# Kernel tuning notes

Hardware: AMD Instinct MI355X
Metric: run time of the kernel (lower is better)

The kernel has to match this reference:

```python
import jax, jax.numpy as jnp
import numpy as np

P = 16  # patch_size

def setup_inputs() -> dict:
    key = jax.random.key(0)
    k1, k2, k3, k4, k5 = jax.random.split(key, 5)
    B, C, H, W = 8, 256, 256, 256
    x = jax.random.normal(k1, (B, C, H, W), dtype=jnp.float32)
    w1 = jax.random.normal(k2, (C, C), dtype=jnp.float32) * 0.02
    b1 = jax.random.normal(k3, (C,), dtype=jnp.float32) * 0.02
    w2 = jax.random.normal(k4, (C, C), dtype=jnp.float32) * 0.02
    b2 = jax.random.normal(k5, (C,), dtype=jnp.float32) * 0.02
    return {"x": x, "w1": w1, "b1": b1, "w2": w2, "b2": b2}

def reference(x, w1, b1, w2, b2):
    B, C, H, W = x.shape
    h, w = H // P, W // P
    # global feature: mean over all spatial positions -> (B, C)
    gf = jnp.mean(x, axis=(2, 3))
    # local features: per-patch mean -> (B, C, h, w)
    lf = jnp.mean(x.reshape(B, C, h, P, w, P), axis=(3, 5))
    lf = lf.reshape(B, C, h * w).transpose(0, 2, 1)  # (B, hw, C)
    mix = jnp.concatenate([lf, gf[:, None, :]], axis=1)  # (B, hw+1, C)
    m = jax.nn.relu(jnp.einsum('bnc,oc->bno', mix, w1) + b1)
    m = jax.nn.relu(jnp.einsum('bnc,oc->bno', m, w2) + b2)
    lf2, gf2 = m[:, :-1, :], m[:, -1, :]  # (B, hw, C), (B, C)
    scores = jnp.einsum('bnc,bc->bn', lf2, gf2)  # (B, hw)
    att = jax.nn.softmax(scores, axis=1).reshape(B, 1, h, w)
    # upsample attention over each patch (nearest / block-broadcast)
    att_up = jnp.repeat(jnp.repeat(att, P, axis=2), P, axis=3)  # (B,1,H,W)
    return x + x * att_up
```

## Files before the change

### kernel.cpp

```cpp
#include <hip/hip_runtime.h>
#include <hip/hip_bf16.h>

typedef float f32x4 __attribute__((ext_vector_type(4)));

#define WS_W1T 0
#define WS_W2T 65536
#define WS_MIX 131072
#define WS_M2  657408
#define WS_ATT 1183744

__global__ void k_transpose(const float* __restrict__ w1,
                            const float* __restrict__ w2,
                            float* __restrict__ w1t,
                            float* __restrict__ w2t) {
    int t = blockIdx.x * 256 + threadIdx.x;
    int idx = t & 65535;
    int o = idx >> 8, c = idx & 255;
    if (t < 65536) w1t[c * 256 + o] = w1[idx];
    else           w2t[c * 256 + o] = w2[idx];
}

__global__ void k_patch_means(const float* __restrict__ x,
                              float* __restrict__ mix) {
    int plane = blockIdx.x;
    int b = plane >> 8, c = plane & 255;
    const f32x4* p = (const f32x4*)x + (size_t)plane * 16384;
    int t = threadIdx.x;
    int lane = t & 63, wid = t >> 6;
    int pcol = lane >> 2;

    __shared__ float bins[16][16];

    const f32x4* wp = p + (size_t)wid * 64 * 64 + lane;
    for (int band = 0; band < 4; ++band) {
        float acc = 0.f;
        #pragma unroll
        for (int r = 0; r < 16; ++r) {
            f32x4 v = __builtin_nontemporal_load(wp + (band * 16 + r) * 64);
            acc += v.x + v.y + v.z + v.w;
        }
        acc += __shfl_xor(acc, 1);
        acc += __shfl_xor(acc, 2);
        if ((lane & 3) == 0) bins[wid * 4 + band][pcol] = acc;
    }
    __syncthreads();

    float pm = bins[t >> 4][t & 15] * (1.0f / 256.0f);
    mix[((size_t)b * 257 + t) * 256 + c] = pm;

    float s = pm;
    for (int off = 1; off < 64; off <<= 1) s += __shfl_xor(s, off);
    __shared__ float wsum[4];
    if (lane == 0) wsum[wid] = s;
    __syncthreads();
    if (t == 0) {
        float g = (wsum[0] + wsum[1] + wsum[2] + wsum[3]) * (1.0f / 256.0f);
        mix[((size_t)b * 257 + 256) * 256 + c] = g;
    }
}

__global__ void k_mlp(const float* __restrict__ mix,
                      const float* __restrict__ w1t, const float* __restrict__ b1,
                      const float* __restrict__ w2t, const float* __restrict__ b2,
                      float* __restrict__ m2out) {
    int r0 = blockIdx.x * 4;
    int o = threadIdx.x;

    __shared__ float in[4][256];
    __shared__ float mid[4][256];
    #pragma unroll
    for (int j = 0; j < 4; ++j) in[j][o] = mix[(size_t)(r0 + j) * 256 + o];
    __syncthreads();

    float acc[4];
    float bb = b1[o];
    #pragma unroll
    for (int j = 0; j < 4; ++j) acc[j] = bb;
    #pragma unroll 4
    for (int c = 0; c < 256; ++c) {
        float wv = w1t[c * 256 + o];
        #pragma unroll
        for (int j = 0; j < 4; ++j) acc[j] = fmaf(in[j][c], wv, acc[j]);
    }
    #pragma unroll
    for (int j = 0; j < 4; ++j) mid[j][o] = fmaxf(acc[j], 0.f);
    __syncthreads();

    float bb2 = b2[o];
    #pragma unroll
    for (int j = 0; j < 4; ++j) acc[j] = bb2;
    #pragma unroll 4
    for (int c = 0; c < 256; ++c) {
        float wv = w2t[c * 256 + o];
        #pragma unroll
        for (int j = 0; j < 4; ++j) acc[j] = fmaf(mid[j][c], wv, acc[j]);
    }
    #pragma unroll
    for (int j = 0; j < 4; ++j)
        m2out[(size_t)(r0 + j) * 256 + o] = fmaxf(acc[j], 0.f);
}

__global__ void k_softmax(const float* __restrict__ m2,
                          float* __restrict__ att) {
    int b = blockIdx.x;
    const float* base = m2 + (size_t)b * 257 * 256;
    int t = threadIdx.x;
    int lane = t & 63, w = t >> 6;

    __shared__ float gf2[256];
    __shared__ float scores[256];
    if (t < 256) gf2[t] = base[65536 + t];
    __syncthreads();

    f32x4 gv = ((const f32x4*)gf2)[lane];
    for (int r = 0; r < 16; ++r) {
        int n = w * 16 + r;
        f32x4 v = ((const f32x4*)(base + (size_t)n * 256))[lane];
        float s = v.x * gv.x + v.y * gv.y + v.z * gv.z + v.w * gv.w;
        #pragma unroll
        for (int off = 1; off < 64; off <<= 1) s += __shfl_xor(s, off);
        if (lane == 0) scores[n] = s;
    }
    __syncthreads();

    float s = (t < 256) ? scores[t] : -1e30f;
    float m = s;
    #pragma unroll
    for (int off = 1; off < 64; off <<= 1) m = fmaxf(m, __shfl_xor(m, off));
    __shared__ float redm[16];
    if (lane == 0) redm[w] = m;
    __syncthreads();
    float M = fmaxf(fmaxf(redm[0], redm[1]), fmaxf(redm[2], redm[3]));

    float e = (t < 256) ? __expf(s - M) : 0.f;
    float sum = e;
    #pragma unroll
    for (int off = 1; off < 64; off <<= 1) sum += __shfl_xor(sum, off);
    __shared__ float reds[16];
    if (lane == 0) reds[w] = sum;
    __syncthreads();
    float S = reds[0] + reds[1] + reds[2] + reds[3];

    if (t < 256) att[b * 256 + t] = e / S;
}

__global__ void k_apply(const float* __restrict__ x,
                        const float* __restrict__ att,
                        float* __restrict__ out) {
    const f32x4* xv = (const f32x4*)x;
    f32x4* ov = (f32x4*)out;
    size_t base = (size_t)blockIdx.x * 1024 + threadIdx.x;
    #pragma unroll
    for (int k = 0; k < 4; ++k) {
        size_t i = base + (size_t)k * 256;
        int plane = (int)(i >> 14);
        int j = (int)(i & 16383);
        int row = j >> 6, col4 = j & 63;
        int patch = ((row >> 4) << 4) | (col4 >> 2);
        int b = plane >> 8;
        float a = 1.0f + att[(b << 8) + patch];
        f32x4 v = __builtin_nontemporal_load(&xv[i]);
        v.x *= a; v.y *= a; v.z *= a; v.w *= a;
        __builtin_nontemporal_store(v, &ov[i]);
    }
}

extern "C" void kernel_launch(void* const* d_in, const int* in_sizes, int n_in,
                              void* d_out, int out_size, void* d_ws, size_t ws_size,
                              hipStream_t stream) {
    const float* x  = (const float*)d_in[0];
    const float* w1 = (const float*)d_in[1];
    const float* b1 = (const float*)d_in[2];
    const float* w2 = (const float*)d_in[3];
    const float* b2 = (const float*)d_in[4];
    float* out = (float*)d_out;
    float* ws  = (float*)d_ws;

    float* w1t = ws + WS_W1T;
    float* w2t = ws + WS_W2T;
    float* mix = ws + WS_MIX;
    float* m2  = ws + WS_M2;
    float* att = ws + WS_ATT;

    k_transpose<<<512, 256, 0, stream>>>(w1, w2, w1t, w2t);
    k_patch_means<<<8 * 256, 256, 0, stream>>>(x, mix);
    k_mlp<<<(8 * 257) / 4, 256, 0, stream>>>(mix, w1t, b1, w2t, b2, m2);
    k_softmax<<<8, 1024, 0, stream>>>(m2, att);
    k_apply<<<32768, 256, 0, stream>>>(x, att, out);
}
```

Baseline: 315.4 us.

## Fuse weight transpose into patch-mean kernel, reverse plane order for cache reuse

Merges the weight-transpose kernel into the patch-means kernel as extra blocks, which removes one launch. The patch-means pass now walks planes in reverse order and uses normal (cached) loads instead of nontemporal ones. The goal is for the last planes read to stay resident in the MI355X's large last-level cache so the apply kernel, which reads x from the start, can hit them. k_apply also computes its attention index once per block because each block covers one patch row, and it drops the nontemporal load on x. The risk is that the reverse order does not match the apply access order well, or that cached reads evict other useful data.

```diff
diff --git a/kernel.cpp b/kernel.cpp
--- a/kernel.cpp
+++ b/kernel.cpp
@@ -9,20 +9,22 @@
 #define WS_M2  657408
 #define WS_ATT 1183744
 
-__global__ void k_transpose(const float* __restrict__ w1,
-                            const float* __restrict__ w2,
-                            float* __restrict__ w1t,
-                            float* __restrict__ w2t) {
-    int t = blockIdx.x * 256 + threadIdx.x;
-    int idx = t & 65535;
-    int o = idx >> 8, c = idx & 255;
-    if (t < 65536) w1t[c * 256 + o] = w1[idx];
-    else           w2t[c * 256 + o] = w2[idx];
-}
-
-__global__ void k_patch_means(const float* __restrict__ x,
-                              float* __restrict__ mix) {
-    int plane = blockIdx.x;
+__global__ void k_means_tr(const float* __restrict__ x,
+                           float* __restrict__ mix,
+                           const float* __restrict__ w1,
+                           const float* __restrict__ w2,
+                           float* __restrict__ w1t,
+                           float* __restrict__ w2t) {
+    int blk = blockIdx.x;
+    if (blk >= 2048) {
+        int t = (blk - 2048) * 256 + threadIdx.x;
+        int idx = t & 65535;
+        int o = idx >> 8, c = idx & 255;
+        if (t < 65536) w1t[c * 256 + o] = w1[idx];
+        else           w2t[c * 256 + o] = w2[idx];
+        return;
+    }
+    int plane = 2047 - blk;
     int b = plane >> 8, c = plane & 255;
     const f32x4* p = (const f32x4*)x + (size_t)plane * 16384;
     int t = threadIdx.x;
@@ -36,7 +38,7 @@
         float acc = 0.f;
         #pragma unroll
         for (int r = 0; r < 16; ++r) {
-            f32x4 v = __builtin_nontemporal_load(wp + (band * 16 + r) * 64);
+            f32x4 v = wp[(band * 16 + r) * 64];
             acc += v.x + v.y + v.z + v.w;
         }
         acc += __shfl_xor(acc, 1);
@@ -149,17 +151,18 @@
                         float* __restrict__ out) {
     const f32x4* xv = (const f32x4*)x;
     f32x4* ov = (f32x4*)out;
-    size_t base = (size_t)blockIdx.x * 1024 + threadIdx.x;
+    int blk = blockIdx.x;
+    int b = blk >> 12;
+    int prow = blk & 15;
+    int col4 = threadIdx.x & 63;
+    int patch = (prow << 4) | (col4 >> 2);
+    float a = 1.0f + att[(b << 8) + patch];
+
+    size_t base = (size_t)blk * 1024 + threadIdx.x;
     #pragma unroll
     for (int k = 0; k < 4; ++k) {
         size_t i = base + (size_t)k * 256;
-        int plane = (int)(i >> 14);
-        int j = (int)(i & 16383);
-        int row = j >> 6, col4 = j & 63;
-        int patch = ((row >> 4) << 4) | (col4 >> 2);
-        int b = plane >> 8;
-        float a = 1.0f + att[(b << 8) + patch];
-        f32x4 v = __builtin_nontemporal_load(&xv[i]);
+        f32x4 v = xv[i];
         v.x *= a; v.y *= a; v.z *= a; v.w *= a;
         __builtin_nontemporal_store(v, &ov[i]);
     }
@@ -182,8 +185,7 @@
     float* m2  = ws + WS_M2;
     float* att = ws + WS_ATT;
 
-    k_transpose<<<512, 256, 0, stream>>>(w1, w2, w1t, w2t);
-    k_patch_means<<<8 * 256, 256, 0, stream>>>(x, mix);
+    k_means_tr<<<2560, 256, 0, stream>>>(x, mix, w1, w2, w1t, w2t);
     k_mlp<<<(8 * 257) / 4, 256, 0, stream>>>(mix, w1t, b1, w2t, b2, m2);
     k_softmax<<<8, 1024, 0, stream>>>(m2, att);
     k_apply<<<32768, 256, 0, stream>>>(x, att, out);
```

After: 321.1 us. About the same (+1.8%).

## Fuse all stages into one persistent kernel with grid-wide barriers

Applied to the files above, without the earlier changes.

Replaces five separate launches (weight transpose, patch means, MLP, softmax, apply) with one persistent kernel sized to occupancy. The stages are separated by atomic-counter grid barriers, and a memset resets the counter each call. The intent is to remove launch gaps and tail effects between stages. The cost is that the tiny softmax stage runs on only 8 blocks while the other blocks spin at a barrier. The final apply pass now caches each batch's attention row in shared memory and walks whole planes per block.

```diff
diff --git a/kernel.cpp b/kernel.cpp
--- a/kernel.cpp
+++ b/kernel.cpp
@@ -8,30 +8,31 @@
 #define WS_MIX 131072
 #define WS_M2  657408
 #define WS_ATT 1183744
-
-__global__ void k_transpose(const float* __restrict__ w1,
-                            const float* __restrict__ w2,
-                            float* __restrict__ w1t,
-                            float* __restrict__ w2t) {
-    int t = blockIdx.x * 256 + threadIdx.x;
-    int idx = t & 65535;
-    int o = idx >> 8, c = idx & 255;
-    if (t < 65536) w1t[c * 256 + o] = w1[idx];
-    else           w2t[c * 256 + o] = w2[idx];
-}
-
-__global__ void k_patch_means(const float* __restrict__ x,
-                              float* __restrict__ mix) {
-    int plane = blockIdx.x;
-    int b = plane >> 8, c = plane & 255;
-    const f32x4* p = (const f32x4*)x + (size_t)plane * 16384;
-    int t = threadIdx.x;
+#define WS_CNT 1185792
+
+__device__ __forceinline__ void grid_bar(unsigned* cnt, unsigned target) {
+    __syncthreads();
+    if (threadIdx.x == 0) {
+        __threadfence();
+        __hip_atomic_fetch_add(cnt, 1u, __ATOMIC_ACQ_REL, __HIP_MEMORY_SCOPE_AGENT);
+        while (__hip_atomic_load(cnt, __ATOMIC_ACQUIRE, __HIP_MEMORY_SCOPE_AGENT) < target) {
+            __builtin_amdgcn_s_sleep(2);
+        }
+        __threadfence();
+    }
+    __syncthreads();
+}
+
+__device__ __forceinline__ void do_plane_means(const float* __restrict__ x,
+                                               float* __restrict__ mix,
+                                               int plane, int t, float* smem) {
     int lane = t & 63, wid = t >> 6;
     int pcol = lane >> 2;
-
-    __shared__ float bins[16][16];
-
-    const f32x4* wp = p + (size_t)wid * 64 * 64 + lane;
+    float (*bins)[16] = (float (*)[16])smem;
+    float* wsum = smem + 256;
+    int b = plane >> 8, c = plane & 255;
+    const f32x4* wp = (const f32x4*)x + (size_t)plane * 16384
+                      + (size_t)wid * 4096 + lane;
     for (int band = 0; band < 4; ++band) {
         float acc = 0.f;
         #pragma unroll
@@ -44,34 +45,30 @@
         if ((lane & 3) == 0) bins[wid * 4 + band][pcol] = acc;
     }
     __syncthreads();
-
     float pm = bins[t >> 4][t & 15] * (1.0f / 256.0f);
     mix[((size_t)b * 257 + t) * 256 + c] = pm;
-
     float s = pm;
     for (int off = 1; off < 64; off <<= 1) s += __shfl_xor(s, off);
-    __shared__ float wsum[4];
     if (lane == 0) wsum[wid] = s;
     __syncthreads();
-    if (t == 0) {
-        float g = (wsum[0] + wsum[1] + wsum[2] + wsum[3]) * (1.0f / 256.0f);
-        mix[((size_t)b * 257 + 256) * 256 + c] = g;
-    }
-}
-
-__global__ void k_mlp(const float* __restrict__ mix,
-                      const float* __restrict__ w1t, const float* __restrict__ b1,
-                      const float* __restrict__ w2t, const float* __restrict__ b2,
-                      float* __restrict__ m2out) {
-    int r0 = blockIdx.x * 4;
-    int o = threadIdx.x;
-
-    __shared__ float in[4][256];
-    __shared__ float mid[4][256];
+    if (t == 0)
+        mix[((size_t)b * 257 + 256) * 256 + c] =
+            (wsum[0] + wsum[1] + wsum[2] + wsum[3]) * (1.0f / 256.0f);
+    __syncthreads();
+}
+
+__device__ __forceinline__ void do_mlp4(const float* __restrict__ mix,
+                                        const float* __restrict__ w1t,
+                                        const float* __restrict__ b1,
+                                        const float* __restrict__ w2t,
+                                        const float* __restrict__ b2,
+                                        float* __restrict__ m2,
+                                        int r0, int o, float* smem) {
+    float (*in)[256]  = (float (*)[256])smem;
+    float (*mid)[256] = (float (*)[256])(smem + 1024);
     #pragma unroll
     for (int j = 0; j < 4; ++j) in[j][o] = mix[(size_t)(r0 + j) * 256 + o];
     __syncthreads();
-
     float acc[4];
     float bb = b1[o];
     #pragma unroll
@@ -85,7 +82,6 @@
     #pragma unroll
     for (int j = 0; j < 4; ++j) mid[j][o] = fmaxf(acc[j], 0.f);
     __syncthreads();
-
     float bb2 = b2[o];
     #pragma unroll
     for (int j = 0; j < 4; ++j) acc[j] = bb2;
@@ -97,24 +93,24 @@
     }
     #pragma unroll
     for (int j = 0; j < 4; ++j)
-        m2out[(size_t)(r0 + j) * 256 + o] = fmaxf(acc[j], 0.f);
-}
-
-__global__ void k_softmax(const float* __restrict__ m2,
-                          float* __restrict__ att) {
-    int b = blockIdx.x;
+        m2[(size_t)(r0 + j) * 256 + o] = fmaxf(acc[j], 0.f);
+    __syncthreads();
+}
+
+__device__ __forceinline__ void do_softmax(const float* __restrict__ m2,
+                                           float* __restrict__ att,
+                                           int b, int t, float* smem) {
     const float* base = m2 + (size_t)b * 257 * 256;
-    int t = threadIdx.x;
-    int lane = t & 63, w = t >> 6;
-
-    __shared__ float gf2[256];
-    __shared__ float scores[256];
-    if (t < 256) gf2[t] = base[65536 + t];
-    __syncthreads();
-
+    int lane = t & 63, wid = t >> 6;
+    float* gf2    = smem;
+    float* scores = smem + 256;
+    float* redm   = smem + 512;
+    float* reds   = smem + 516;
+    gf2[t] = base[65536 + t];
+    __syncthreads();
     f32x4 gv = ((const f32x4*)gf2)[lane];
-    for (int r = 0; r < 16; ++r) {
-        int n = w * 16 + r;
+    for (int r = 0; r < 64; ++r) {
+        int n = wid * 64 + r;
         f32x4 v = ((const f32x4*)(base + (size_t)n * 256))[lane];
         float s = v.x * gv.x + v.y * gv.y + v.z * gv.z + v.w * gv.w;
         #pragma unroll
@@ -122,46 +118,94 @@
         if (lane == 0) scores[n] = s;
     }
     __syncthreads();
-
-    float s = (t < 256) ? scores[t] : -1e30f;
+    float s = scores[t];
     float m = s;
     #pragma unroll
     for (int off = 1; off < 64; off <<= 1) m = fmaxf(m, __shfl_xor(m, off));
-    __shared__ float redm[16];
-    if (lane == 0) redm[w] = m;
+    if (lane == 0) redm[wid] = m;
     __syncthreads();
     float M = fmaxf(fmaxf(redm[0], redm[1]), fmaxf(redm[2], redm[3]));
-
-    float e = (t < 256) ? __expf(s - M) : 0.f;
+    float e = __expf(s - M);
     float sum = e;
     #pragma unroll
     for (int off = 1; off < 64; off <<= 1) sum += __shfl_xor(sum, off);
-    __shared__ float reds[16];
-    if (lane == 0) reds[w] = sum;
+    if (lane == 0) reds[wid] = sum;
     __syncthreads();
     float S = reds[0] + reds[1] + reds[2] + reds[3];
-
-    if (t < 256) att[b * 256 + t] = e / S;
-}
-
-__global__ void k_apply(const float* __restrict__ x,
-                        const float* __restrict__ att,
-                        float* __restrict__ out) {
-    const f32x4* xv = (const f32x4*)x;
-    f32x4* ov = (f32x4*)out;
-    size_t base = (size_t)blockIdx.x * 1024 + threadIdx.x;
-    #pragma unroll
-    for (int k = 0; k < 4; ++k) {
-        size_t i = base + (size_t)k * 256;
-        int plane = (int)(i >> 14);
-        int j = (int)(i & 16383);
-        int row = j >> 6, col4 = j & 63;
-        int patch = ((row >> 4) << 4) | (col4 >> 2);
+    att[b * 256 + t] = e / S;
+    __syncthreads();
+}
+
+__device__ __forceinline__ void do_apply_plane(const float* __restrict__ x,
+                                               float* __restrict__ out,
+                                               const float* __restrict__ att_l,
+                                               int plane, int t) {
+    const f32x4* xv = (const f32x4*)x + (size_t)plane * 16384;
+    f32x4* ov = (f32x4*)out + (size_t)plane * 16384;
+    int col4 = t & 63;
+    #pragma unroll 4
+    for (int prow = 0; prow < 16; ++prow) {
+        float a = 1.0f + att_l[(prow << 4) | (col4 >> 2)];
+        size_t base2 = (size_t)prow * 1024 + t;
+        #pragma unroll
+        for (int k = 0; k < 4; ++k) {
+            size_t i = base2 + (size_t)k * 256;
+            f32x4 v = __builtin_nontemporal_load(&xv[i]);
+            v.x *= a; v.y *= a; v.z *= a; v.w *= a;
+            __builtin_nontemporal_store(v, &ov[i]);
+        }
+    }
+}
+
+__global__ void __launch_bounds__(256, 4) k_fused(
+    const float* __restrict__ x,
+    const float* __restrict__ w1, const float* __restrict__ b1,
+    const float* __restrict__ w2, const float* __restrict__ b2,
+    float* __restrict__ out, float* __restrict__ ws, int NB)
+{
+    float* w1t = ws + WS_W1T;
+    float* w2t = ws + WS_W2T;
+    float* mix = ws + WS_MIX;
+    float* m2  = ws + WS_M2;
+    float* att = ws + WS_ATT;
+    unsigned* cnt = (unsigned*)(ws + WS_CNT);
+
+    int blk = blockIdx.x;
+    int t = threadIdx.x;
+    __shared__ float smem[2064];
+
+    for (int idx = blk * 256 + t; idx < 131072; idx += NB * 256) {
+        int m = idx & 65535;
+        int o = m >> 8, c = m & 255;
+        if (idx < 65536) w1t[c * 256 + o] = w1[m];
+        else             w2t[c * 256 + o] = w2[m];
+    }
+    for (int plane = blk; plane < 2048; plane += NB)
+        do_plane_means(x, mix, plane, t, smem);
+
+    grid_bar(cnt, (unsigned)NB);
+
+    for (int vb = blk; vb < 514; vb += NB)
+        do_mlp4(mix, w1t, b1, w2t, b2, m2, vb * 4, t, smem);
+
+    grid_bar(cnt, (unsigned)(2 * NB));
+
+    for (int vb = blk; vb < 8; vb += NB)
+        do_softmax(m2, att, vb, t, smem);
+
+    grid_bar(cnt, (unsigned)(3 * NB));
+
+    float* att_l = smem;
+    int cur_b = -1;
+    for (int plane = blk; plane < 2048; plane += NB) {
         int b = plane >> 8;
-        float a = 1.0f + att[(b << 8) + patch];
-        f32x4 v = __builtin_nontemporal_load(&xv[i]);
-        v.x *= a; v.y *= a; v.z *= a; v.w *= a;
-        __builtin_nontemporal_store(v, &ov[i]);
+        if (b != cur_b) {
+            __syncthreads();
+            att_l[t] = att[b * 256 + t];
+            __syncthreads();
+            cur_b = b;
+        }
+        do_apply_plane(x, out, att_l, plane, t);
     }
 }
 
@@ -176,15 +220,14 @@
     float* out = (float*)d_out;
     float* ws  = (float*)d_ws;
 
-    float* w1t = ws + WS_W1T;
-    float* w2t = ws + WS_W2T;
-    float* mix = ws + WS_MIX;
-    float* m2  = ws + WS_M2;
-    float* att = ws + WS_ATT;
-
-    k_transpose<<<512, 256, 0, stream>>>(w1, w2, w1t, w2t);
-    k_patch_means<<<8 * 256, 256, 0, stream>>>(x, mix);
-    k_mlp<<<(8 * 257) / 4, 256, 0, stream>>>(mix, w1t, b1, w2t, b2, m2);
-    k_softmax<<<8, 1024, 0, stream>>>(m2, att);
-    k_apply<<<32768, 256, 0, stream>>>(x, att, out);
-}
+    int perCU = 0;
+    hipError_t e = hipOccupancyMaxActiveBlocksPerMultiprocessor(
+        &perCU, (const void*)k_fused, 256, 0);
+    if (e != hipSuccess || perCU < 1) perCU = 1;
+    int NB = perCU * 256;
+    if (NB > 2048) NB = 2048;
+
+    hipMemsetAsync(ws + WS_CNT, 0, 64, stream);
+
+    k_fused<<<NB, 256, 0, stream>>>(x, w1, b1, w2, b2, out, ws, NB);
+}
```

Result: slower. 808.8 us (+156.4%).
